# Performance work log

Hardware: AMD Instinct MI355X
Metric: run time of the kernel (lower is better)

## Reference

```python
import jax, jax.numpy as jnp
import numpy as np

N_GENE, N_DRUG = 20000, 3000
D_GENE, D_DRUG = 1024, 512
H = [256, 128]
E_GG, E_DD, E_DT = 600000, 120000, 150000
P_DROP = 0.2


def _dropout(x, key):
    # F.dropout(p=0.2, training=True) with a fixed key for determinism
    keep = jax.random.bernoulli(key, 1.0 - P_DROP, x.shape)
    return jnp.where(keep, x / (1.0 - P_DROP), 0.0).astype(x.dtype)


def _gcn_norm(x, W, b, edge_index, n):
    src, dst = edge_index[0], edge_index[1]
    loops = jnp.arange(n, dtype=src.dtype)
    src = jnp.concatenate([src, loops])
    dst = jnp.concatenate([dst, loops])
    deg = jax.ops.segment_sum(jnp.ones(src.shape, x.dtype), dst, num_segments=n)
    dinv = jax.lax.rsqrt(deg)  # deg >= 1 thanks to self loops
    xw = x @ W  # [n_src, out]
    msg = xw[src] * (dinv[src] * dinv[dst])[:, None]  # [E+n, out]
    return jax.ops.segment_sum(msg, dst, num_segments=n) + b


def _gcn_plain(x, W, b, edge_index, n_dst):
    # PyG GCNConv(add_self_loops=False, normalize=False): A X W + b (bipartite scatter)
    xw = x @ W
    return jax.ops.segment_sum(xw[edge_index[0]], edge_index[1], num_segments=n_dst) + b


def _l2norm(x):
    # F.normalize(dim=1, p=2), eps=1e-12
    n = jnp.linalg.norm(x, axis=1, keepdims=True)
    return x / jnp.maximum(n, 1e-12)


def setup_inputs() -> dict:
    key = jax.random.key(0)
    ks = jax.random.split(key, 32)
    inp = {}
    inp["gene_feat"] = jax.random.normal(ks[0], (N_GENE, D_GENE), jnp.float32)
    inp["drug_feat"] = jax.random.normal(ks[1], (N_DRUG, D_DRUG), jnp.float32)
    inp["ei_gg"] = jax.random.randint(ks[2], (2, E_GG), 0, N_GENE)
    inp["ei_dd"] = jax.random.randint(ks[3], (2, E_DD), 0, N_DRUG)
    # drug_target: messages from drug (src row) to gene (dst row)
    inp["ei_dt"] = jnp.stack([jax.random.randint(ks[4], (E_DT,), 0, N_DRUG),
                               jax.random.randint(ks[5], (E_DT,), 0, N_GENE)])
    # target_drug: messages from gene (src row) to drug (dst row)
    inp["ei_td"] = jnp.stack([jax.random.randint(ks[6], (E_DT,), 0, N_GENE),
                               jax.random.randint(ks[7], (E_DT,), 0, N_DRUG)])
    dims_in = {"gg": D_GENE, "dd": D_DRUG, "dt": D_DRUG, "td": D_GENE}
    i = 8
    for l, h in enumerate(H):
        for et in ["gg", "dd", "dt", "td"]:
            din = dims_in[et] if l == 0 else H[l - 1]
            s = float(1.0 / np.sqrt(din))
            inp[f"W{l}_{et}"] = jax.random.uniform(ks[i], (din, h), jnp.float32, -s, s)
            i += 1
            inp[f"b{l}_{et}"] = jnp.zeros((h,), jnp.float32)
    return inp


def reference(gene_feat, drug_feat, ei_gg, ei_dd, ei_dt, ei_td,
              W0_gg, b0_gg, W0_dd, b0_dd, W0_dt, b0_dt, W0_td, b0_td,
              W1_gg, b1_gg, W1_dd, b1_dd, W1_dt, b1_dt, W1_td, b1_td):
    dk = jax.random.split(jax.random.key(42), 8)
    layers = [
        ((W0_gg, b0_gg), (W0_dd, b0_dd), (W0_dt, b0_dt), (W0_td, b0_td)),
        ((W1_gg, b1_gg), (W1_dd, b1_dd), (W1_dt, b1_dt), (W1_td, b1_td)),
    ]
    xg, xd = gene_feat, drug_feat
    k = 0
    for (Wgg, bgg), (Wdd, bdd), (Wdt, bdt), (Wtd, btd) in layers:
        gg = jax.nn.relu(_gcn_norm(_dropout(xg, dk[k + 0]), Wgg, bgg, ei_gg, N_GENE))
        dd = jax.nn.relu(_gcn_norm(_dropout(xd, dk[k + 1]), Wdd, bdd, ei_dd, N_DRUG))
        dt = jax.nn.relu(_gcn_plain(_dropout(xd, dk[k + 2]), Wdt, bdt, ei_dt, N_GENE))
        td = jax.nn.relu(_gcn_plain(_dropout(xg, dk[k + 3]), Wtd, btd, ei_td, N_DRUG))
        # per-edge-type L2 normalize, then sum contributions per node type
        xg = _l2norm(gg) + _l2norm(dt)
        xd = _l2norm(dd) + _l2norm(td)
        k += 4
    # concat node-type outputs: genes first, drugs second -> [N_GENE+N_DRUG, H[-1]]
    return jnp.concatenate([xg, xd], axis=0)
```

## Files before the change

### kernel.cpp

```cpp
#include <hip/hip_runtime.h>
#include <stdint.h>

#define N_GENE 20000
#define N_DRUG 3000
#define D_GENE 1024
#define D_DRUG 512
#define H0 256
#define H1 128
#define E_GG 600000
#define E_DD 120000
#define E_DT 150000

typedef __attribute__((ext_vector_type(8))) short bf16x8;
typedef __attribute__((ext_vector_type(4))) float f32x4;

__host__ __device__ inline uint32_t rotl32(uint32_t x, int d) {
    return (x << d) | (x >> (32 - d));
}

__host__ __device__ inline void tf2x32(uint32_t k0, uint32_t k1, uint32_t x0, uint32_t x1,
                                       uint32_t& o0, uint32_t& o1) {
    uint32_t ks2 = k0 ^ k1 ^ 0x1BD11BDAu;
    x0 += k0; x1 += k1;
#define TFR(r) { x0 += x1; x1 = rotl32(x1, r); x1 ^= x0; }
    TFR(13) TFR(15) TFR(26) TFR(6)
    x0 += k1; x1 += ks2 + 1u;
    TFR(17) TFR(29) TFR(16) TFR(24)
    x0 += ks2; x1 += k0 + 2u;
    TFR(13) TFR(15) TFR(26) TFR(6)
    x0 += k0; x1 += k1 + 3u;
    TFR(17) TFR(29) TFR(16) TFR(24)
    x0 += k1; x1 += ks2 + 4u;
    TFR(13) TFR(15) TFR(26) TFR(6)
    x0 += ks2; x1 += k0 + 5u;
#undef TFR
    o0 = x0; o1 = x1;
}

__device__ inline short f2bf(float f) {
    uint32_t u = __float_as_uint(f);
    uint32_t r = (u + 0x7FFFu + ((u >> 16) & 1u)) >> 16;
    return (short)r;
}
__device__ inline float bf_lo(uint32_t u) { return __uint_as_float(u << 16); }
__device__ inline float bf_hi(uint32_t u) { return __uint_as_float(u & 0xFFFF0000u); }

struct Cast4P {
    unsigned c0, c1, c2, c3;
    uint32_t k0a, k1a, k0b, k1b, k0c, k1c, k0d, k1d;
};
__global__ __launch_bounds__(256) void cast4_kernel(const float* __restrict__ Xg,
                                                    const float* __restrict__ Xd,
                                                    short* __restrict__ Am, Cast4P P) {
    unsigned j = (blockIdx.x * 256u + threadIdx.x) * 8u;
    if (j >= P.c3) return;
    unsigned base; uint32_t k0, k1; const float* X;
    if (j >= P.c2)      { base = P.c2; k0 = P.k0d; k1 = P.k1d; X = Xd; }
    else if (j >= P.c1) { base = P.c1; k0 = P.k0c; k1 = P.k1c; X = Xd; }
    else if (j >= P.c0) { base = P.c0; k0 = P.k0b; k1 = P.k1b; X = Xg; }
    else                { base = 0u;   k0 = P.k0a; k1 = P.k1a; X = Xg; }
    unsigned local = j - base;
    float4 xa = *(const float4*)(X + local);
    float4 xb = *(const float4*)(X + local + 4);
    float xv[8] = {xa.x, xa.y, xa.z, xa.w, xb.x, xb.y, xb.z, xb.w};
    union { short s[8]; uint4 u; } st;
#pragma unroll
    for (int i = 0; i < 8; i++) {
        uint32_t a, b;
        tf2x32(k0, k1, 0u, local + (unsigned)i, a, b);
        uint32_t bits = a ^ b;
        st.s[i] = ((bits >> 9) < 6710887u) ? f2bf(xv[i] * 1.25f) : (short)0;
    }
    *(uint4*)(Am + j) = st.u;
}

struct CastT4P {
    unsigned c0, c1, c2, c3;
    int lgK0, lgK1, lgK2, lgK3;
    int N;
};
__global__ __launch_bounds__(256) void castT4_kernel(
    const float* __restrict__ W0, const float* __restrict__ W1,
    const float* __restrict__ W2, const float* __restrict__ W3,
    short* __restrict__ Wt, CastT4P P) {
    unsigned idx = blockIdx.x * 256u + threadIdx.x;
    if (idx >= P.c3) return;
    unsigned base; const float* W; int lgK;
    if (idx >= P.c2)      { base = P.c2; W = W3; lgK = P.lgK3; }
    else if (idx >= P.c1) { base = P.c1; W = W2; lgK = P.lgK2; }
    else if (idx >= P.c0) { base = P.c0; W = W1; lgK = P.lgK1; }
    else                  { base = 0u;   W = W0; lgK = P.lgK0; }
    unsigned local = idx - base;
    unsigned n = local >> lgK, k = local & ((1u << lgK) - 1u);
    Wt[idx] = f2bf(W[(size_t)k * P.N + n]);
}

struct GDesc { unsigned aoff, boff, coff; const float* rs; int M, K, mb0; };
#define LDP 72
__global__ __launch_bounds__(256) void gemm4_kernel(
    const short* __restrict__ Ab, const short* __restrict__ Wb, short* __restrict__ Cb,
    GDesc d0, GDesc d1, GDesc d2, GDesc d3, int N) {
    __shared__ short As[64 * LDP];
    __shared__ short Bs[64 * LDP];
    GDesc d;
    int bx = blockIdx.x;
    if (bx >= d3.mb0) d = d3;
    else if (bx >= d2.mb0) d = d2;
    else if (bx >= d1.mb0) d = d1;
    else d = d0;
    bx -= d.mb0;
    const short* A = Ab + d.aoff;
    const short* Bt = Wb + d.boff;
    short* C = Cb + d.coff;
    const int M = d.M, K = d.K;

    int tid = threadIdx.x;
    int lane = tid & 63;
    int w = tid >> 6;
    int m = lane & 15, kb = lane >> 4;
    int m0w = (w >> 1) * 32, n0w = (w & 1) * 32;
    int gm = bx * 64, gn = blockIdx.y * 64;

    int flat0 = tid, flat1 = tid + 256;
    int ar0 = flat0 >> 3, ac0 = (flat0 & 7) * 8;
    int ar1 = flat1 >> 3, ac1 = (flat1 & 7) * 8;
    int agr0 = min(gm + ar0, M - 1), agr1 = min(gm + ar1, M - 1);
    const short* pa0 = A + (size_t)agr0 * K + ac0;
    const short* pa1 = A + (size_t)agr1 * K + ac1;
    const short* pb0 = Bt + (size_t)(gn + ar0) * K + ac0;
    const short* pb1 = Bt + (size_t)(gn + ar1) * K + ac1;

    f32x4 acc[2][2];
#pragma unroll
    for (int i = 0; i < 2; i++)
#pragma unroll
        for (int j = 0; j < 2; j++) acc[i][j] = (f32x4){0.f, 0.f, 0.f, 0.f};

    uint4 ra0 = *(const uint4*)pa0;
    uint4 ra1 = *(const uint4*)pa1;
    uint4 rb0 = *(const uint4*)pb0;
    uint4 rb1 = *(const uint4*)pb1;

    int nt = K >> 6;
    for (int t = 0; t < nt; ++t) {
        __syncthreads();
        *(uint4*)&As[ar0 * LDP + ac0] = ra0;
        *(uint4*)&As[ar1 * LDP + ac1] = ra1;
        *(uint4*)&Bs[ar0 * LDP + ac0] = rb0;
        *(uint4*)&Bs[ar1 * LDP + ac1] = rb1;
        __syncthreads();
        if (t + 1 < nt) {
            int kt = (t + 1) << 6;
            ra0 = *(const uint4*)(pa0 + kt);
            ra1 = *(const uint4*)(pa1 + kt);
            rb0 = *(const uint4*)(pb0 + kt);
            rb1 = *(const uint4*)(pb1 + kt);
        }
#pragma unroll
        for (int ks = 0; ks < 2; ++ks) {
            bf16x8 a0 = *(const bf16x8*)&As[(m0w + m) * LDP + ks * 32 + kb * 8];
            bf16x8 a1 = *(const bf16x8*)&As[(m0w + 16 + m) * LDP + ks * 32 + kb * 8];
            bf16x8 b0 = *(const bf16x8*)&Bs[(n0w + m) * LDP + ks * 32 + kb * 8];
            bf16x8 b1 = *(const bf16x8*)&Bs[(n0w + 16 + m) * LDP + ks * 32 + kb * 8];
            acc[0][0] = __builtin_amdgcn_mfma_f32_16x16x32_bf16(a0, b0, acc[0][0], 0, 0, 0);
            acc[0][1] = __builtin_amdgcn_mfma_f32_16x16x32_bf16(a0, b1, acc[0][1], 0, 0, 0);
            acc[1][0] = __builtin_amdgcn_mfma_f32_16x16x32_bf16(a1, b0, acc[1][0], 0, 0, 0);
            acc[1][1] = __builtin_amdgcn_mfma_f32_16x16x32_bf16(a1, b1, acc[1][1], 0, 0, 0);
        }
    }
#pragma unroll
    for (int mf = 0; mf < 2; ++mf)
#pragma unroll
        for (int j = 0; j < 4; ++j) {
            int r = gm + m0w + mf * 16 + kb * 4 + j;
            if (r < M) {
                float s = d.rs ? d.rs[r] : 1.0f;
#pragma unroll
                for (int nf = 0; nf < 2; ++nf)
                    C[(size_t)r * N + gn + n0w + nf * 16 + m] = f2bf(acc[mf][nf][j] * s);
            }
        }
}

#define CUM_E0 600000u
#define CUM_E1 720000u
#define CUM_E2 870000u
#define CUM_E3 1020000u

__global__ void count4_kernel(const int* __restrict__ gg, const int* __restrict__ dd,
                              const int* __restrict__ dt, const int* __restrict__ td,
                              int* __restrict__ cnt) {
    unsigned e = blockIdx.x * 256u + threadIdx.x;
    if (e >= CUM_E3) return;
    const int* dsts; unsigned base, noff;
    if (e >= CUM_E2)      { dsts = td + E_DT; base = CUM_E2; noff = 43000; }
    else if (e >= CUM_E1) { dsts = dt + E_DT; base = CUM_E1; noff = 23000; }
    else if (e >= CUM_E0) { dsts = dd + E_DD; base = CUM_E0; noff = 20000; }
    else                  { dsts = gg + E_GG; base = 0;      noff = 0; }
    atomicAdd(&cnt[noff + dsts[e - base]], 1);
}

__global__ void scan4_kernel(const int* __restrict__ cnt,
                             int* __restrict__ rp0, int* __restrict__ rp1,
                             int* __restrict__ rp2, int* __restrict__ rp3) {
    __shared__ int buf[1024];
    __shared__ int carry_s;
    const int ns[4]   = {20000, 3000, 20000, 3000};
    const int offs[4] = {0, 20000, 23000, 43000};
    int b = blockIdx.x;
    int n = ns[b];
    const int* c = cnt + offs[b];
    int* rowptr = (b == 0) ? rp0 : (b == 1) ? rp1 : (b == 2) ? rp2 : rp3;
    int tid = threadIdx.x;
    if (tid == 0) carry_s = 0;
    __syncthreads();
    for (int base = 0; base < n; base += 1024) {
        int i = base + tid;
        int v = (i < n) ? c[i] : 0;
        buf[tid] = v;
        __syncthreads();
        for (int off = 1; off < 1024; off <<= 1) {
            int t = (tid >= off) ? buf[tid - off] : 0;
            __syncthreads();
            if (tid >= off) buf[tid] += t;
            __syncthreads();
        }
        int incl = buf[tid];
        int cc = carry_s;
        __syncthreads();
        if (i < n) rowptr[i] = cc + incl - v;
        if (tid == 1023) carry_s = cc + buf[1023];
        __syncthreads();
    }
    if (tid == 0) rowptr[n] = carry_s;
}

__global__ void copy4_kernel(const int* __restrict__ rp0, const int* __restrict__ rp1,
                             const int* __restrict__ rp2, const int* __restrict__ rp3,
                             int* __restrict__ pos) {
    unsigned i = blockIdx.x * 256u + threadIdx.x;
    if (i >= 46000u) return;
    int v;
    if (i >= 43000u) v = rp3[i - 43000u];
    else if (i >= 23000u) v = rp2[i - 23000u];
    else if (i >= 20000u) v = rp1[i - 20000u];
    else v = rp0[i];
    pos[i] = v;
}

__global__ void fill4_kernel(const int* __restrict__ gg, const int* __restrict__ dd,
                             const int* __restrict__ dt, const int* __restrict__ td,
                             int* __restrict__ pos, int* __restrict__ col) {
    unsigned e = blockIdx.x * 256u + threadIdx.x;
    if (e >= CUM_E3) return;
    const int* ei; unsigned base, noff, coff; int E;
    if (e >= CUM_E2)      { ei = td; base = CUM_E2; noff = 43000; coff = 870000; E = E_DT; }
    else if (e >= CUM_E1) { ei = dt; base = CUM_E1; noff = 23000; coff = 720000; E = E_DT; }
    else if (e >= CUM_E0) { ei = dd; base = CUM_E0; noff = 20000; coff = 600000; E = E_DD; }
    else                  { ei = gg; base = 0;      noff = 0;     coff = 0;      E = E_GG; }
    unsigned local = e - base;
    int src = ei[local], dst = ei[E + local];
    int p = atomicAdd(&pos[noff + dst], 1);
    col[coff + p] = src;
}

__global__ void dinv2_kernel(const int* __restrict__ cnt, float* __restrict__ dinv_g,
                             float* __restrict__ dinv_d) {
    unsigned i = blockIdx.x * 256u + threadIdx.x;
    if (i >= 23000u) return;
    if (i < 20000u) dinv_g[i] = 1.0f / sqrtf((float)cnt[i] + 1.0f);
    else dinv_d[i - 20000u] = 1.0f / sqrtf((float)cnt[i] + 1.0f);
}

template <int F>
__global__ __launch_bounds__(256) void agg2_kernel(
    const short* __restrict__ XWa, const int* __restrict__ rpa, const int* __restrict__ cola,
    const float* __restrict__ dinv, const float* __restrict__ ba,
    const short* __restrict__ XWb2, const int* __restrict__ rpb, const int* __restrict__ colb,
    const float* __restrict__ bb, float* __restrict__ out, int n_dst) {
    const int h = 64 * F;
    int lane = threadIdx.x & 63;
    int row = blockIdx.x * 4 + (threadIdx.x >> 6);
    if (row >= n_dst) return;
    int c0 = lane * F;
    float acc[F], va[F];

#pragma unroll
    for (int i = 0; i < F; i++) acc[i] = 0.f;
    {
        if constexpr (F == 4) {
            uint2 u = *(const uint2*)(XWa + (size_t)row * h + c0);
            acc[0] += bf_lo(u.x); acc[1] += bf_hi(u.x);
            acc[2] += bf_lo(u.y); acc[3] += bf_hi(u.y);
        } else {
            uint32_t u = *(const uint32_t*)(XWa + (size_t)row * h + c0);
            acc[0] += bf_lo(u); acc[1] += bf_hi(u);
        }
        int s0 = rpa[row], s1 = rpa[row + 1];
        int p = s0;
        for (; p + 8 <= s1; p += 8) {
            int c[8];
#pragma unroll
            for (int i = 0; i < 8; i++) c[i] = cola[p + i];
            if constexpr (F == 4) {
                uint2 g[8];
#pragma unroll
                for (int i = 0; i < 8; i++) g[i] = *(const uint2*)(XWa + (size_t)c[i] * h + c0);
#pragma unroll
                for (int i = 0; i < 8; i++) {
                    acc[0] += bf_lo(g[i].x); acc[1] += bf_hi(g[i].x);
                    acc[2] += bf_lo(g[i].y); acc[3] += bf_hi(g[i].y);
                }
            } else {
                uint32_t g[8];
#pragma unroll
                for (int i = 0; i < 8; i++) g[i] = *(const uint32_t*)(XWa + (size_t)c[i] * h + c0);
#pragma unroll
                for (int i = 0; i < 8; i++) { acc[0] += bf_lo(g[i]); acc[1] += bf_hi(g[i]); }
            }
        }
        for (; p < s1; p++) {
            int s = cola[p];
            if constexpr (F == 4) {
                uint2 u = *(const uint2*)(XWa + (size_t)s * h + c0);
                acc[0] += bf_lo(u.x); acc[1] += bf_hi(u.x);
                acc[2] += bf_lo(u.y); acc[3] += bf_hi(u.y);
            } else {
                uint32_t u = *(const uint32_t*)(XWa + (size_t)s * h + c0);
                acc[0] += bf_lo(u); acc[1] += bf_hi(u);
            }
        }
    }
    float mul = dinv[row];
    float ssa = 0.f;
#pragma unroll
    for (int i = 0; i < F; i++) {
        float v = fmaxf(acc[i] * mul + ba[c0 + i], 0.f);
        va[i] = v;
        ssa += v * v;
    }

#pragma unroll
    for (int i = 0; i < F; i++) acc[i] = 0.f;
    {
        int s0 = rpb[row], s1 = rpb[row + 1];
        int p = s0;
        for (; p + 8 <= s1; p += 8) {
            int c[8];
#pragma unroll
            for (int i = 0; i < 8; i++) c[i] = colb[p + i];
            if constexpr (F == 4) {
                uint2 g[8];
#pragma unroll
                for (int i = 0; i < 8; i++) g[i] = *(const uint2*)(XWb2 + (size_t)c[i] * h + c0);
#pragma unroll
                for (int i = 0; i < 8; i++) {
                    acc[0] += bf_lo(g[i].x); acc[1] += bf_hi(g[i].x);
                    acc[2] += bf_lo(g[i].y); acc[3] += bf_hi(g[i].y);
                }
            } else {
                uint32_t g[8];
#pragma unroll
                for (int i = 0; i < 8; i++) g[i] = *(const uint32_t*)(XWb2 + (size_t)c[i] * h + c0);
#pragma unroll
                for (int i = 0; i < 8; i++) { acc[0] += bf_lo(g[i]); acc[1] += bf_hi(g[i]); }
            }
        }
        for (; p < s1; p++) {
            int s = colb[p];
            if constexpr (F == 4) {
                uint2 u = *(const uint2*)(XWb2 + (size_t)s * h + c0);
                acc[0] += bf_lo(u.x); acc[1] += bf_hi(u.x);
                acc[2] += bf_lo(u.y); acc[3] += bf_hi(u.y);
            } else {
                uint32_t u = *(const uint32_t*)(XWb2 + (size_t)s * h + c0);
                acc[0] += bf_lo(u); acc[1] += bf_hi(u);
            }
        }
    }
    float ssb = 0.f;
#pragma unroll
    for (int i = 0; i < F; i++) {
        float v = fmaxf(acc[i] + bb[c0 + i], 0.f);
        acc[i] = v;
        ssb += v * v;
    }

#pragma unroll
    for (int off = 32; off >= 1; off >>= 1) {
        ssa += __shfl_xor(ssa, off, 64);
        ssb += __shfl_xor(ssb, off, 64);
    }
    float sa = 1.0f / fmaxf(sqrtf(ssa), 1e-12f);
    float sb = 1.0f / fmaxf(sqrtf(ssb), 1e-12f);
    float* orow = out + (size_t)row * h + c0;
    if constexpr (F == 4) {
        *(float4*)orow = make_float4(va[0] * sa + acc[0] * sb, va[1] * sa + acc[1] * sb,
                                     va[2] * sa + acc[2] * sb, va[3] * sa + acc[3] * sb);
    } else {
        *(float2*)orow = make_float2(va[0] * sa + acc[0] * sb, va[1] * sa + acc[1] * sb);
    }
}

extern "C" void kernel_launch(void* const* d_in, const int* in_sizes, int n_in,
                              void* d_out, int out_size, void* d_ws, size_t ws_size,
                              hipStream_t stream) {
    const float* gene = (const float*)d_in[0];
    const float* drug = (const float*)d_in[1];
    const int* ei_gg = (const int*)d_in[2];
    const int* ei_dd = (const int*)d_in[3];
    const int* ei_dt = (const int*)d_in[4];
    const int* ei_td = (const int*)d_in[5];
    const float* W0gg = (const float*)d_in[6];  const float* b0gg = (const float*)d_in[7];
    const float* W0dd = (const float*)d_in[8];  const float* b0dd = (const float*)d_in[9];
    const float* W0dt = (const float*)d_in[10]; const float* b0dt = (const float*)d_in[11];
    const float* W0td = (const float*)d_in[12]; const float* b0td = (const float*)d_in[13];
    const float* W1gg = (const float*)d_in[14]; const float* b1gg = (const float*)d_in[15];
    const float* W1dd = (const float*)d_in[16]; const float* b1dd = (const float*)d_in[17];
    const float* W1dt = (const float*)d_in[18]; const float* b1dt = (const float*)d_in[19];
    const float* W1td = (const float*)d_in[20]; const float* b1td = (const float*)d_in[21];

    uint32_t dk[8][2];
    for (uint32_t i = 0; i < 8; i++) tf2x32(0u, 42u, 0u, i, dk[i][0], dk[i][1]);

    char* p = (char*)d_ws;
    auto take = [&](size_t bytes) -> void* {
        void* r = (void*)p;
        p += (bytes + 255) & ~(size_t)255;
        return r;
    };
    short* Am   = (short*)take(sizeof(short) * 44032000ULL);
    short* XW   = (short*)take(sizeof(short) * 11776000ULL);
    short* Wt   = (short*)take(sizeof(short) * 786432ULL);
    float* xg1  = (float*)take(sizeof(float) * (size_t)N_GENE * H0);
    float* xd1  = (float*)take(sizeof(float) * (size_t)N_DRUG * H0);
    float* dinv_g = (float*)take(sizeof(float) * N_GENE);
    float* dinv_d = (float*)take(sizeof(float) * N_DRUG);
    int* cnt = (int*)take(4 * 46000);
    int* pos = (int*)take(4 * 46000);
    int* col = (int*)take(4 * 1020000);
    int* rp_gg = (int*)take(4 * (N_GENE + 1));
    int* rp_dd = (int*)take(4 * (N_DRUG + 1));
    int* rp_dt = (int*)take(4 * (N_GENE + 1));
    int* rp_td = (int*)take(4 * (N_DRUG + 1));

    hipMemsetAsync(cnt, 0, 4 * 46000, stream);
    count4_kernel<<<(1020000 + 255) / 256, 256, 0, stream>>>(ei_gg, ei_dd, ei_dt, ei_td, cnt);
    scan4_kernel<<<4, 1024, 0, stream>>>(cnt, rp_gg, rp_dd, rp_dt, rp_td);
    copy4_kernel<<<(46000 + 255) / 256, 256, 0, stream>>>(rp_gg, rp_dd, rp_dt, rp_td, pos);
    fill4_kernel<<<(1020000 + 255) / 256, 256, 0, stream>>>(ei_gg, ei_dd, ei_dt, ei_td, pos, col);
    dinv2_kernel<<<(23000 + 255) / 256, 256, 0, stream>>>(cnt, dinv_g, dinv_d);

    const int* col_gg = col;
    const int* col_dd = col + 600000;
    const int* col_dt = col + 720000;
    const int* col_td = col + 870000;

    {
        Cast4P cp = {20480000u, 40960000u, 42496000u, 44032000u,
                     dk[0][0], dk[0][1], dk[3][0], dk[3][1],
                     dk[1][0], dk[1][1], dk[2][0], dk[2][1]};
        cast4_kernel<<<(44032000 / 8 + 255) / 256, 256, 0, stream>>>(gene, drug, Am, cp);
        CastT4P tp = {262144u, 524288u, 655360u, 786432u, 10, 10, 9, 9, H0};
        castT4_kernel<<<(786432 + 255) / 256, 256, 0, stream>>>(W0gg, W0td, W0dd, W0dt, Wt, tp);
        GDesc g0 = {0u,         0u,       0u,         dinv_g, N_GENE, 1024, 0};
        GDesc g1 = {20480000u,  262144u,  5120000u,   nullptr, N_GENE, 1024, 313};
        GDesc g2 = {40960000u,  524288u,  10240000u,  dinv_d, N_DRUG, 512, 626};
        GDesc g3 = {42496000u,  655360u,  11008000u,  nullptr, N_DRUG, 512, 673};
        gemm4_kernel<<<dim3(720, H0 / 64), 256, 0, stream>>>(Am, Wt, XW, g0, g1, g2, g3, H0);
        agg2_kernel<4><<<(N_GENE + 3) / 4, 256, 0, stream>>>(
            XW, rp_gg, col_gg, dinv_g, b0gg,
            XW + 11008000, rp_dt, col_dt, b0dt, xg1, N_GENE);
        agg2_kernel<4><<<(N_DRUG + 3) / 4, 256, 0, stream>>>(
            XW + 10240000, rp_dd, col_dd, dinv_d, b0dd,
            XW + 5120000, rp_td, col_td, b0td, xd1, N_DRUG);
    }

    {
        Cast4P cp = {5120000u, 10240000u, 11008000u, 11776000u,
                     dk[4][0], dk[4][1], dk[7][0], dk[7][1],
                     dk[5][0], dk[5][1], dk[6][0], dk[6][1]};
        cast4_kernel<<<(11776000 / 8 + 255) / 256, 256, 0, stream>>>(xg1, xd1, Am, cp);
        CastT4P tp = {32768u, 65536u, 98304u, 131072u, 8, 8, 8, 8, H1};
        castT4_kernel<<<(131072 + 255) / 256, 256, 0, stream>>>(W1gg, W1td, W1dd, W1dt, Wt, tp);
        GDesc g0 = {0u,         0u,      0u,         dinv_g, N_GENE, 256, 0};
        GDesc g1 = {5120000u,   32768u,  5120000u,   nullptr, N_GENE, 256, 313};
        GDesc g2 = {10240000u,  65536u,  10240000u,  dinv_d, N_DRUG, 256, 626};
        GDesc g3 = {11008000u,  98304u,  11008000u,  nullptr, N_DRUG, 256, 673};
        gemm4_kernel<<<dim3(720, H1 / 64), 256, 0, stream>>>(Am, Wt, XW, g0, g1, g2, g3, H1);
        float* og = (float*)d_out;
        float* od = og + (size_t)N_GENE * H1;
        agg2_kernel<2><<<(N_GENE + 3) / 4, 256, 0, stream>>>(
            XW, rp_gg, col_gg, dinv_g, b1gg,
            XW + 11008000, rp_dt, col_dt, b1dt, og, N_GENE);
        agg2_kernel<2><<<(N_DRUG + 3) / 4, 256, 0, stream>>>(
            XW + 10240000, rp_dd, col_dd, dinv_d, b1dd,
            XW + 5120000, rp_td, col_td, b1td, od, N_DRUG);
    }
}
```

Baseline: 464.7 us.

## Fuse CSR build into cast kernels and parallelize scan across blocks

Folds the edge-count atomics into the layer-0 dropout/cast launch and the CSR fill into the weight-transpose launch. The single-block-per-type serial scan becomes a three-phase multi-block scan over one global rowptr array that also writes pos and dinv, so the copy and dinv kernels go away. Aggregation now indexes one global col array, and rotl uses the alignbit intrinsic. This cuts launches and the serialized scan, at the cost of more branching inside the merged kernels.

```diff
diff --git a/kernel.cpp b/kernel.cpp
--- a/kernel.cpp
+++ b/kernel.cpp
@@ -15,7 +15,11 @@
 typedef __attribute__((ext_vector_type(4))) float f32x4;
 
 __host__ __device__ inline uint32_t rotl32(uint32_t x, int d) {
+#ifdef __HIP_DEVICE_COMPILE__
+    return __builtin_amdgcn_alignbit(x, x, 32 - d);
+#else
     return (x << d) | (x >> (32 - d));
+#endif
 }
 
 __host__ __device__ inline void tf2x32(uint32_t k0, uint32_t k1, uint32_t x0, uint32_t x1,
@@ -45,14 +49,33 @@
 __device__ inline float bf_lo(uint32_t u) { return __uint_as_float(u << 16); }
 __device__ inline float bf_hi(uint32_t u) { return __uint_as_float(u & 0xFFFF0000u); }
 
+#define CUM_E0 600000u
+#define CUM_E1 720000u
+#define CUM_E2 870000u
+#define CUM_E3 1020000u
+
 struct Cast4P {
     unsigned c0, c1, c2, c3;
     uint32_t k0a, k1a, k0b, k1b, k0c, k1c, k0d, k1d;
 };
-__global__ __launch_bounds__(256) void cast4_kernel(const float* __restrict__ Xg,
-                                                    const float* __restrict__ Xd,
-                                                    short* __restrict__ Am, Cast4P P) {
-    unsigned j = (blockIdx.x * 256u + threadIdx.x) * 8u;
+__global__ __launch_bounds__(256) void cast4_kernel(
+    const float* __restrict__ Xg, const float* __restrict__ Xd,
+    short* __restrict__ Am, Cast4P P, int castBlocks,
+    const int* __restrict__ gg, const int* __restrict__ dd,
+    const int* __restrict__ dt, const int* __restrict__ td, int* __restrict__ cnt) {
+    int bx = blockIdx.x;
+    if (bx >= castBlocks) {
+        unsigned e = (unsigned)(bx - castBlocks) * 256u + threadIdx.x;
+        if (e >= CUM_E3) return;
+        const int* dsts; unsigned base, noff;
+        if (e >= CUM_E2)      { dsts = td + E_DT; base = CUM_E2; noff = 43000; }
+        else if (e >= CUM_E1) { dsts = dt + E_DT; base = CUM_E1; noff = 23000; }
+        else if (e >= CUM_E0) { dsts = dd + E_DD; base = CUM_E0; noff = 20000; }
+        else                  { dsts = gg + E_GG; base = 0;      noff = 0; }
+        atomicAdd(&cnt[noff + dsts[e - base]], 1);
+        return;
+    }
+    unsigned j = ((unsigned)bx * 256u + threadIdx.x) * 8u;
     if (j >= P.c3) return;
     unsigned base; uint32_t k0, k1; const float* X;
     if (j >= P.c2)      { base = P.c2; k0 = P.k0d; k1 = P.k1d; X = Xd; }
@@ -74,11 +97,91 @@
     *(uint4*)(Am + j) = st.u;
 }
 
+__global__ __launch_bounds__(1024) void scan_p1(const int* __restrict__ cnt,
+                                                int* __restrict__ tmp, int* __restrict__ bsum) {
+    __shared__ int buf[1024];
+    int tid = threadIdx.x;
+    int i = blockIdx.x * 1024 + tid;
+    int v = (i < 46000) ? cnt[i] : 0;
+    buf[tid] = v;
+    __syncthreads();
+    for (int off = 1; off < 1024; off <<= 1) {
+        int t = (tid >= off) ? buf[tid - off] : 0;
+        __syncthreads();
+        buf[tid] += t;
+        __syncthreads();
+    }
+    if (i < 46000) tmp[i] = buf[tid];
+    if (tid == 1023) bsum[blockIdx.x] = buf[1023];
+}
+
+__global__ void scan_p2(int* __restrict__ bsum) {
+    int lane = threadIdx.x;
+    int v = (lane < 45) ? bsum[lane] : 0;
+    int orig = v;
+    for (int off = 1; off < 64; off <<= 1) {
+        int t = __shfl_up(v, off, 64);
+        if (lane >= off) v += t;
+    }
+    if (lane < 45) bsum[lane] = v - orig;
+}
+
+__global__ __launch_bounds__(1024) void scan_p3(const int* __restrict__ cnt,
+                                                const int* __restrict__ tmp,
+                                                const int* __restrict__ bsum,
+                                                int* __restrict__ rpall, int* __restrict__ pos,
+                                                float* __restrict__ dinv_g,
+                                                float* __restrict__ dinv_d) {
+    int i = blockIdx.x * 1024 + threadIdx.x;
+    if (i < 46000) {
+        int g = tmp[i] - cnt[i] + bsum[blockIdx.x];
+        rpall[i] = g;
+        pos[i] = g;
+        if (i < 20000) dinv_g[i] = 1.0f / sqrtf((float)cnt[i] + 1.0f);
+        else if (i < 23000) dinv_d[i - 20000] = 1.0f / sqrtf((float)cnt[i] + 1.0f);
+    }
+    if (i == 0) rpall[46000] = (int)CUM_E3;
+}
+
 struct CastT4P {
     unsigned c0, c1, c2, c3;
     int lgK0, lgK1, lgK2, lgK3;
     int N;
 };
+__global__ __launch_bounds__(256) void fillcastT_kernel(
+    const int* __restrict__ gg, const int* __restrict__ dd,
+    const int* __restrict__ dt, const int* __restrict__ td,
+    int* __restrict__ pos, int* __restrict__ col,
+    const float* __restrict__ W0, const float* __restrict__ W1,
+    const float* __restrict__ W2, const float* __restrict__ W3,
+    short* __restrict__ Wt, CastT4P P, int fillBlocks) {
+    int bx = blockIdx.x;
+    if (bx < fillBlocks) {
+        unsigned e = (unsigned)bx * 256u + threadIdx.x;
+        if (e >= CUM_E3) return;
+        const int* ei; unsigned base, noff; int E;
+        if (e >= CUM_E2)      { ei = td; base = CUM_E2; noff = 43000; E = E_DT; }
+        else if (e >= CUM_E1) { ei = dt; base = CUM_E1; noff = 23000; E = E_DT; }
+        else if (e >= CUM_E0) { ei = dd; base = CUM_E0; noff = 20000; E = E_DD; }
+        else                  { ei = gg; base = 0;      noff = 0;     E = E_GG; }
+        unsigned local = e - base;
+        int src = ei[local], dst = ei[E + local];
+        int p = atomicAdd(&pos[noff + dst], 1);
+        col[p] = src;
+        return;
+    }
+    unsigned idx = (unsigned)(bx - fillBlocks) * 256u + threadIdx.x;
+    if (idx >= P.c3) return;
+    unsigned base; const float* W; int lgK;
+    if (idx >= P.c2)      { base = P.c2; W = W3; lgK = P.lgK3; }
+    else if (idx >= P.c1) { base = P.c1; W = W2; lgK = P.lgK2; }
+    else if (idx >= P.c0) { base = P.c0; W = W1; lgK = P.lgK1; }
+    else                  { base = 0u;   W = W0; lgK = P.lgK0; }
+    unsigned local = idx - base;
+    unsigned n = local >> lgK, k = local & ((1u << lgK) - 1u);
+    Wt[idx] = f2bf(W[(size_t)k * P.N + n]);
+}
+
 __global__ __launch_bounds__(256) void castT4_kernel(
     const float* __restrict__ W0, const float* __restrict__ W1,
     const float* __restrict__ W2, const float* __restrict__ W3,
@@ -182,102 +285,13 @@
         }
 }
 
-#define CUM_E0 600000u
-#define CUM_E1 720000u
-#define CUM_E2 870000u
-#define CUM_E3 1020000u
-
-__global__ void count4_kernel(const int* __restrict__ gg, const int* __restrict__ dd,
-                              const int* __restrict__ dt, const int* __restrict__ td,
-                              int* __restrict__ cnt) {
-    unsigned e = blockIdx.x * 256u + threadIdx.x;
-    if (e >= CUM_E3) return;
-    const int* dsts; unsigned base, noff;
-    if (e >= CUM_E2)      { dsts = td + E_DT; base = CUM_E2; noff = 43000; }
-    else if (e >= CUM_E1) { dsts = dt + E_DT; base = CUM_E1; noff = 23000; }
-    else if (e >= CUM_E0) { dsts = dd + E_DD; base = CUM_E0; noff = 20000; }
-    else                  { dsts = gg + E_GG; base = 0;      noff = 0; }
-    atomicAdd(&cnt[noff + dsts[e - base]], 1);
-}
-
-__global__ void scan4_kernel(const int* __restrict__ cnt,
-                             int* __restrict__ rp0, int* __restrict__ rp1,
-                             int* __restrict__ rp2, int* __restrict__ rp3) {
-    __shared__ int buf[1024];
-    __shared__ int carry_s;
-    const int ns[4]   = {20000, 3000, 20000, 3000};
-    const int offs[4] = {0, 20000, 23000, 43000};
-    int b = blockIdx.x;
-    int n = ns[b];
-    const int* c = cnt + offs[b];
-    int* rowptr = (b == 0) ? rp0 : (b == 1) ? rp1 : (b == 2) ? rp2 : rp3;
-    int tid = threadIdx.x;
-    if (tid == 0) carry_s = 0;
-    __syncthreads();
-    for (int base = 0; base < n; base += 1024) {
-        int i = base + tid;
-        int v = (i < n) ? c[i] : 0;
-        buf[tid] = v;
-        __syncthreads();
-        for (int off = 1; off < 1024; off <<= 1) {
-            int t = (tid >= off) ? buf[tid - off] : 0;
-            __syncthreads();
-            if (tid >= off) buf[tid] += t;
-            __syncthreads();
-        }
-        int incl = buf[tid];
-        int cc = carry_s;
-        __syncthreads();
-        if (i < n) rowptr[i] = cc + incl - v;
-        if (tid == 1023) carry_s = cc + buf[1023];
-        __syncthreads();
-    }
-    if (tid == 0) rowptr[n] = carry_s;
-}
-
-__global__ void copy4_kernel(const int* __restrict__ rp0, const int* __restrict__ rp1,
-                             const int* __restrict__ rp2, const int* __restrict__ rp3,
-                             int* __restrict__ pos) {
-    unsigned i = blockIdx.x * 256u + threadIdx.x;
-    if (i >= 46000u) return;
-    int v;
-    if (i >= 43000u) v = rp3[i - 43000u];
-    else if (i >= 23000u) v = rp2[i - 23000u];
-    else if (i >= 20000u) v = rp1[i - 20000u];
-    else v = rp0[i];
-    pos[i] = v;
-}
-
-__global__ void fill4_kernel(const int* __restrict__ gg, const int* __restrict__ dd,
-                             const int* __restrict__ dt, const int* __restrict__ td,
-                             int* __restrict__ pos, int* __restrict__ col) {
-    unsigned e = blockIdx.x * 256u + threadIdx.x;
-    if (e >= CUM_E3) return;
-    const int* ei; unsigned base, noff, coff; int E;
-    if (e >= CUM_E2)      { ei = td; base = CUM_E2; noff = 43000; coff = 870000; E = E_DT; }
-    else if (e >= CUM_E1) { ei = dt; base = CUM_E1; noff = 23000; coff = 720000; E = E_DT; }
-    else if (e >= CUM_E0) { ei = dd; base = CUM_E0; noff = 20000; coff = 600000; E = E_DD; }
-    else                  { ei = gg; base = 0;      noff = 0;     coff = 0;      E = E_GG; }
-    unsigned local = e - base;
-    int src = ei[local], dst = ei[E + local];
-    int p = atomicAdd(&pos[noff + dst], 1);
-    col[coff + p] = src;
-}
-
-__global__ void dinv2_kernel(const int* __restrict__ cnt, float* __restrict__ dinv_g,
-                             float* __restrict__ dinv_d) {
-    unsigned i = blockIdx.x * 256u + threadIdx.x;
-    if (i >= 23000u) return;
-    if (i < 20000u) dinv_g[i] = 1.0f / sqrtf((float)cnt[i] + 1.0f);
-    else dinv_d[i - 20000u] = 1.0f / sqrtf((float)cnt[i] + 1.0f);
-}
-
 template <int F>
 __global__ __launch_bounds__(256) void agg2_kernel(
-    const short* __restrict__ XWa, const int* __restrict__ rpa, const int* __restrict__ cola,
+    const short* __restrict__ XWa, const int* __restrict__ rpa,
     const float* __restrict__ dinv, const float* __restrict__ ba,
-    const short* __restrict__ XWb2, const int* __restrict__ rpb, const int* __restrict__ colb,
-    const float* __restrict__ bb, float* __restrict__ out, int n_dst) {
+    const short* __restrict__ XWb2, const int* __restrict__ rpb,
+    const float* __restrict__ bb, const int* __restrict__ col,
+    float* __restrict__ out, int n_dst) {
     const int h = 64 * F;
     int lane = threadIdx.x & 63;
     int row = blockIdx.x * 4 + (threadIdx.x >> 6);
@@ -301,7 +315,7 @@
         for (; p + 8 <= s1; p += 8) {
             int c[8];
 #pragma unroll
-            for (int i = 0; i < 8; i++) c[i] = cola[p + i];
+            for (int i = 0; i < 8; i++) c[i] = col[p + i];
             if constexpr (F == 4) {
                 uint2 g[8];
 #pragma unroll
@@ -320,7 +334,7 @@
             }
         }
         for (; p < s1; p++) {
-            int s = cola[p];
+            int s = col[p];
             if constexpr (F == 4) {
                 uint2 u = *(const uint2*)(XWa + (size_t)s * h + c0);
                 acc[0] += bf_lo(u.x); acc[1] += bf_hi(u.x);
@@ -348,7 +362,7 @@
         for (; p + 8 <= s1; p += 8) {
             int c[8];
 #pragma unroll
-            for (int i = 0; i < 8; i++) c[i] = colb[p + i];
+            for (int i = 0; i < 8; i++) c[i] = col[p + i];
             if constexpr (F == 4) {
                 uint2 g[8];
 #pragma unroll
@@ -367,7 +381,7 @@
             }
         }
         for (; p < s1; p++) {
-            int s = colb[p];
+            int s = col[p];
             if constexpr (F == 4) {
                 uint2 u = *(const uint2*)(XWb2 + (size_t)s * h + c0);
                 acc[0] += bf_lo(u.x); acc[1] += bf_hi(u.x);
@@ -436,65 +450,66 @@
     float* xd1  = (float*)take(sizeof(float) * (size_t)N_DRUG * H0);
     float* dinv_g = (float*)take(sizeof(float) * N_GENE);
     float* dinv_d = (float*)take(sizeof(float) * N_DRUG);
-    int* cnt = (int*)take(4 * 46000);
-    int* pos = (int*)take(4 * 46000);
-    int* col = (int*)take(4 * 1020000);
-    int* rp_gg = (int*)take(4 * (N_GENE + 1));
-    int* rp_dd = (int*)take(4 * (N_DRUG + 1));
-    int* rp_dt = (int*)take(4 * (N_GENE + 1));
-    int* rp_td = (int*)take(4 * (N_DRUG + 1));
+    int* cnt   = (int*)take(4 * 46000);
+    int* tmp   = (int*)take(4 * 46000);
+    int* bsum  = (int*)take(4 * 64);
+    int* pos   = (int*)take(4 * 46000);
+    int* rpall = (int*)take(4 * 46001);
+    int* col   = (int*)take(4 * 1020000);
+
+    const int* rp_gg = rpall;
+    const int* rp_dd = rpall + 20000;
+    const int* rp_dt = rpall + 23000;
+    const int* rp_td = rpall + 43000;
 
     hipMemsetAsync(cnt, 0, 4 * 46000, stream);
-    count4_kernel<<<(1020000 + 255) / 256, 256, 0, stream>>>(ei_gg, ei_dd, ei_dt, ei_td, cnt);
-    scan4_kernel<<<4, 1024, 0, stream>>>(cnt, rp_gg, rp_dd, rp_dt, rp_td);
-    copy4_kernel<<<(46000 + 255) / 256, 256, 0, stream>>>(rp_gg, rp_dd, rp_dt, rp_td, pos);
-    fill4_kernel<<<(1020000 + 255) / 256, 256, 0, stream>>>(ei_gg, ei_dd, ei_dt, ei_td, pos, col);
-    dinv2_kernel<<<(23000 + 255) / 256, 256, 0, stream>>>(cnt, dinv_g, dinv_d);
-
-    const int* col_gg = col;
-    const int* col_dd = col + 600000;
-    const int* col_dt = col + 720000;
-    const int* col_td = col + 870000;
 
     {
         Cast4P cp = {20480000u, 40960000u, 42496000u, 44032000u,
                      dk[0][0], dk[0][1], dk[3][0], dk[3][1],
                      dk[1][0], dk[1][1], dk[2][0], dk[2][1]};
-        cast4_kernel<<<(44032000 / 8 + 255) / 256, 256, 0, stream>>>(gene, drug, Am, cp);
+        int castBlocks = 44032000 / 8 / 256;
+        int countBlocks = (1020000 + 255) / 256;
+        cast4_kernel<<<castBlocks + countBlocks, 256, 0, stream>>>(
+            gene, drug, Am, cp, castBlocks, ei_gg, ei_dd, ei_dt, ei_td, cnt);
+        scan_p1<<<45, 1024, 0, stream>>>(cnt, tmp, bsum);
+        scan_p2<<<1, 64, 0, stream>>>(bsum);
+        scan_p3<<<45, 1024, 0, stream>>>(cnt, tmp, bsum, rpall, pos, dinv_g, dinv_d);
         CastT4P tp = {262144u, 524288u, 655360u, 786432u, 10, 10, 9, 9, H0};
-        castT4_kernel<<<(786432 + 255) / 256, 256, 0, stream>>>(W0gg, W0td, W0dd, W0dt, Wt, tp);
-        GDesc g0 = {0u,         0u,       0u,         dinv_g, N_GENE, 1024, 0};
-        GDesc g1 = {20480000u,  262144u,  5120000u,   nullptr, N_GENE, 1024, 313};
-        GDesc g2 = {40960000u,  524288u,  10240000u,  dinv_d, N_DRUG, 512, 626};
-        GDesc g3 = {42496000u,  655360u,  11008000u,  nullptr, N_DRUG, 512, 673};
+        int fillBlocks = (1020000 + 255) / 256;
+        fillcastT_kernel<<<fillBlocks + (786432 + 255) / 256, 256, 0, stream>>>(
+            ei_gg, ei_dd, ei_dt, ei_td, pos, col,
+            W0gg, W0td, W0dd, W0dt, Wt, tp, fillBlocks);
+        GDesc g0 = {0u,        0u,      0u,        dinv_g,  N_GENE, 1024, 0};
+        GDesc g1 = {20480000u, 262144u, 5120000u,  nullptr, N_GENE, 1024, 313};
+        GDesc g2 = {40960000u, 524288u, 10240000u, dinv_d,  N_DRUG, 512,  626};
+        GDesc g3 = {42496000u, 655360u, 11008000u, nullptr, N_DRUG, 512,  673};
         gemm4_kernel<<<dim3(720, H0 / 64), 256, 0, stream>>>(Am, Wt, XW, g0, g1, g2, g3, H0);
         agg2_kernel<4><<<(N_GENE + 3) / 4, 256, 0, stream>>>(
-            XW, rp_gg, col_gg, dinv_g, b0gg,
-            XW + 11008000, rp_dt, col_dt, b0dt, xg1, N_GENE);
+            XW, rp_gg, dinv_g, b0gg, XW + 11008000, rp_dt, b0dt, col, xg1, N_GENE);
         agg2_kernel<4><<<(N_DRUG + 3) / 4, 256, 0, stream>>>(
-            XW + 10240000, rp_dd, col_dd, dinv_d, b0dd,
-            XW + 5120000, rp_td, col_td, b0td, xd1, N_DRUG);
+            XW + 10240000, rp_dd, dinv_d, b0dd, XW + 5120000, rp_td, b0td, col, xd1, N_DRUG);
     }
 
     {
         Cast4P cp = {5120000u, 10240000u, 11008000u, 11776000u,
                      dk[4][0], dk[4][1], dk[7][0], dk[7][1],
                      dk[5][0], dk[5][1], dk[6][0], dk[6][1]};
-        cast4_kernel<<<(11776000 / 8 + 255) / 256, 256, 0, stream>>>(xg1, xd1, Am, cp);
+        int castBlocks = 11776000 / 8 / 256;
+        cast4_kernel<<<castBlocks, 256, 0, stream>>>(
+            xg1, xd1, Am, cp, castBlocks, nullptr, nullptr, nullptr, nullptr, nullptr);
         CastT4P tp = {32768u, 65536u, 98304u, 131072u, 8, 8, 8, 8, H1};
         castT4_kernel<<<(131072 + 255) / 256, 256, 0, stream>>>(W1gg, W1td, W1dd, W1dt, Wt, tp);
-        GDesc g0 = {0u,         0u,      0u,         dinv_g, N_GENE, 256, 0};
-        GDesc g1 = {5120000u,   32768u,  5120000u,   nullptr, N_GENE, 256, 313};
-        GDesc g2 = {10240000u,  65536u,  10240000u,  dinv_d, N_DRUG, 256, 626};
-        GDesc g3 = {11008000u,  98304u,  11008000u,  nullptr, N_DRUG, 256, 673};
+        GDesc g0 = {0u,        0u,     0u,        dinv_g,  N_GENE, 256, 0};
+        GDesc g1 = {5120000u,  32768u, 5120000u,  nullptr, N_GENE, 256, 313};
+        GDesc g2 = {10240000u, 65536u, 10240000u, dinv_d,  N_DRUG, 256, 626};
+        GDesc g3 = {11008000u, 98304u, 11008000u, nullptr, N_DRUG, 256, 673};
         gemm4_kernel<<<dim3(720, H1 / 64), 256, 0, stream>>>(Am, Wt, XW, g0, g1, g2, g3, H1);
         float* og = (float*)d_out;
         float* od = og + (size_t)N_GENE * H1;
         agg2_kernel<2><<<(N_GENE + 3) / 4, 256, 0, stream>>>(
-            XW, rp_gg, col_gg, dinv_g, b1gg,
-            XW + 11008000, rp_dt, col_dt, b1dt, og, N_GENE);
+            XW, rp_gg, dinv_g, b1gg, XW + 11008000, rp_dt, b1dt, col, og, N_GENE);
         agg2_kernel<2><<<(N_DRUG + 3) / 4, 256, 0, stream>>>(
-            XW + 10240000, rp_dd, col_dd, dinv_d, b1dd,
-            XW + 5120000, rp_td, col_td, b1td, od, N_DRUG);
-    }
-}
+            XW + 10240000, rp_dd, dinv_d, b1dd, XW + 5120000, rp_td, b1td, col, od, N_DRUG);
+    }
+}
```

New measurement: 421.3 us. -9.4%, faster.
